# Kernel optimization log

Hardware: AMD Instinct MI355X
Metric: run time of the kernel (lower is better)

The kernel has to match this reference:

```python
import jax, jax.numpy as jnp
import numpy as np

N = 8192
D_IN = 128
D_HID = 256  # hard-coded nn.Linear(input_dim, 256) in the module
D_OUT = 64
BN_EPS = 1e-5
LEAKY_SLOPE = 0.01


def setup_inputs() -> dict:
    key = jax.random.key(0)
    k_h, k_a, k_wt, k_wo = jax.random.split(key, 4)
    H = jax.random.normal(k_h, (N, D_IN), dtype=jnp.float32)
    # Fixed adjacency passed to __init__; values in [0,1) so mask=ceil(A*1e-5) is {0,1}
    A = jax.random.uniform(k_a, (N, N), dtype=jnp.float32)
    bn_weight = jnp.ones((D_IN,), jnp.float32)
    bn_bias = jnp.zeros((D_IN,), jnp.float32)
    W_theta = jax.random.normal(k_wt, (D_IN, D_HID), jnp.float32) * np.float32(1.0 / np.sqrt(D_IN))
    b_theta = jnp.zeros((D_HID,), jnp.float32)
    W_out = jax.random.normal(k_wo, (D_IN, D_OUT), jnp.float32) * np.float32(1.0 / np.sqrt(D_IN))
    b_out = jnp.zeros((D_OUT,), jnp.float32)
    return {"H": H, "A": A, "bn_weight": bn_weight, "bn_bias": bn_bias,
            "W_theta": W_theta, "b_theta": b_theta, "W_out": W_out, "b_out": b_out}


def reference(H, A, bn_weight, bn_bias, W_theta, b_theta, W_out, b_out):
    # BatchNorm1d in training mode: biased batch statistics over the node dim
    mean = jnp.mean(H, axis=0)
    var = jnp.mean(jnp.square(H - mean), axis=0)
    Hn = (H - mean) * jax.lax.rsqrt(var + BN_EPS) * bn_weight + bn_bias  # [N, D_IN]

    Hx = Hn @ W_theta + b_theta  # [N, 256]
    mask = jnp.ceil(A * 1e-5)    # constant {0,1} mask from fixed adjacency

    # Dynamic adjacency: clamp(sigmoid(Hx Hx^T), min=0.1) * mask + I
    S = jnp.clip(jax.nn.sigmoid(Hx @ Hx.T), 0.1, None)  # [N, N]
    Ad = S * mask + jnp.eye(N, dtype=H.dtype)

    # D^{-1/2} A D^{-1/2} via broadcast scaling (same math as diag matmuls)
    d = jax.lax.rsqrt(jnp.sum(Ad, axis=1))  # D^{-0.5}, [N]
    A_hat = Ad * d[:, None] * d[None, :]

    out = A_hat @ (Hn @ W_out + b_out)       # [N, D_OUT]
    out = jnp.where(out >= 0, out, LEAKY_SLOPE * out)  # LeakyReLU(0.01)
    return out, A_hat
```

## Files before the change

### kernel.cpp

```cpp
#include <hip/hip_runtime.h>
#include <hip/hip_bf16.h>

#define N 8192
#define DIN 128
#define DHID 256
#define DOUT 64
#define LDP 72
#define VP 136

typedef __attribute__((ext_vector_type(8))) short short8;
typedef __attribute__((ext_vector_type(8))) unsigned short u16x8;
typedef __attribute__((ext_vector_type(4))) float f32x4;
typedef __attribute__((ext_vector_type(4))) unsigned short u16x4;

typedef __attribute__((address_space(1))) const unsigned int GlbU32;
typedef __attribute__((address_space(3))) unsigned int LdsU32;

__device__ inline void gload16(const void* g, void* l) {
  __builtin_amdgcn_global_load_lds((GlbU32*)g, (LdsU32*)l, 16, 0, 0);
}

#define LGKM_BAR()                                            \
  do {                                                        \
    asm volatile("s_waitcnt lgkmcnt(0)" ::: "memory");        \
    __builtin_amdgcn_sched_barrier(0);                        \
    __builtin_amdgcn_s_barrier();                             \
    __builtin_amdgcn_sched_barrier(0);                        \
  } while (0)

__device__ inline unsigned short f2bf(float x) {
  unsigned u = __float_as_uint(x);
  u += 0x7FFF + ((u >> 16) & 1);
  return (unsigned short)(u >> 16);
}
__device__ inline float bf2f(unsigned short u) {
  return __uint_as_float(((unsigned)u) << 16);
}
__device__ inline float sig_clip(float x) {
  float s = 1.0f / (1.0f + __expf(-x));
  return fmaxf(s, 0.1f);
}

__global__ __launch_bounds__(256) void maskpack(const float* __restrict__ A,
                                                unsigned long long* __restrict__ Mb) {
  size_t i = (size_t)blockIdx.x * 256 + threadIdx.x;
  size_t step = (size_t)gridDim.x * 256;
  int l = threadIdx.x & 63;
  for (; i < (size_t)N * N / 4; i += step) {
    f32x4 a = *(const f32x4*)&A[i * 4];
    unsigned long long b0 = __ballot(a[0] > 0.f);
    unsigned long long b1 = __ballot(a[1] > 0.f);
    unsigned long long b2 = __ballot(a[2] > 0.f);
    unsigned long long b3 = __ballot(a[3] > 0.f);
    size_t g = (i - l) >> 6;
    if (l < 4) {
      unsigned long long bb = (l == 0) ? b0 : (l == 1) ? b1 : (l == 2) ? b2 : b3;
      Mb[g * 4 + l] = bb;
    }
  }
}

__global__ void bn_stats(const float* __restrict__ H, const float* __restrict__ bnw,
                         const float* __restrict__ bnb, float* __restrict__ scale,
                         float* __restrict__ shift) {
  int f = blockIdx.x;
  int t = threadIdx.x;
  float s = 0.f, sq = 0.f;
  for (int r = t; r < N; r += 256) {
    float v = H[(size_t)r * DIN + f];
    s += v; sq += v * v;
  }
  __shared__ float ss[256], s2[256];
  ss[t] = s; s2[t] = sq;
  __syncthreads();
  for (int o = 128; o > 0; o >>= 1) {
    if (t < o) { ss[t] += ss[t + o]; s2[t] += s2[t + o]; }
    __syncthreads();
  }
  if (t == 0) {
    float mean = ss[0] * (1.0f / N);
    float var = s2[0] * (1.0f / N) - mean * mean;
    float sc = rsqrtf(var + 1e-5f) * bnw[f];
    scale[f] = sc;
    shift[f] = bnb[f] - mean * sc;
  }
}

__global__ __launch_bounds__(256) void proj(const float* __restrict__ H,
                     const float* __restrict__ scale, const float* __restrict__ shift,
                     const float* __restrict__ Wt, const float* __restrict__ bt,
                     const float* __restrict__ Wo, const float* __restrict__ bo,
                     unsigned short* __restrict__ Hx, unsigned short* __restrict__ M2T) {
  __shared__ float hn[8][DIN];
  int i0 = blockIdx.x * 8;
  int t = threadIdx.x;
  #pragma unroll
  for (int rep = 0; rep < 4; ++rep) {
    int idx = rep * 256 + t;
    int r = idx >> 7, c = idx & 127;
    float h = H[(size_t)(i0 + r) * DIN + c];
    hn[r][c] = fmaf(h, scale[c], shift[c]);
  }
  __syncthreads();
  {
    int c = t;
    float acc[8];
    float b = bt[c];
    #pragma unroll
    for (int r = 0; r < 8; ++r) acc[r] = b;
    for (int k = 0; k < DIN; ++k) {
      float w = Wt[k * DHID + c];
      #pragma unroll
      for (int r = 0; r < 8; ++r) acc[r] = fmaf(hn[r][k], w, acc[r]);
    }
    #pragma unroll
    for (int r = 0; r < 8; ++r) Hx[(size_t)(i0 + r) * DHID + c] = f2bf(acc[r]);
  }
  if (t < DOUT) {
    int c = t;
    float acc[8];
    float b = bo[c];
    #pragma unroll
    for (int r = 0; r < 8; ++r) acc[r] = b;
    for (int k = 0; k < DIN; ++k) {
      float w = Wo[k * DOUT + c];
      #pragma unroll
      for (int r = 0; r < 8; ++r) acc[r] = fmaf(hn[r][k], w, acc[r]);
    }
    u16x8 v;
    #pragma unroll
    for (int r = 0; r < 8; ++r) v[r] = f2bf(acc[r]);
    *(u16x8*)&M2T[(size_t)c * N + i0] = v;
  }
}

template <int BF16V>
__global__ __launch_bounds__(256) void smat(const unsigned short* __restrict__ Hx,
                     const unsigned long long* __restrict__ Mb,
                     float* __restrict__ rowsum,
                     void* __restrict__ Vout) {
  __shared__ unsigned short lsh[17408];
  __shared__ unsigned mbt32[128][4];
  unsigned short* la = lsh;
  unsigned short* lb = lsh + 8192;
  int jt = blockIdx.x, it = blockIdx.y;
  int i0 = it * 128, j0 = jt * 128;
  int t = threadIdx.x;
  int w = t >> 6, l = t & 63;
  int lr = l & 15, lg = l >> 4;

  if (t < 128) {
    const unsigned long long* src = &Mb[(size_t)(i0 + t) * (N / 64) + (j0 >> 8) * 4];
    int sh = (j0 & 128) ? 32 : 0;
    #pragma unroll
    for (int e = 0; e < 4; ++e)
      mbt32[t][e] = (unsigned)(src[e] >> sh);
  }

  f32x4 acc[2][8];
  f32x4 zero = {0.f, 0.f, 0.f, 0.f};
  #pragma unroll
  for (int m = 0; m < 2; ++m)
    #pragma unroll
    for (int n = 0; n < 8; ++n) acc[m][n] = zero;

  const int srow = l >> 3;
  const int scol = ((l & 7) ^ srow) * 8;
  const int fswz = (lr & 7) * 8;

  for (int c4 = 0; c4 < 4; ++c4) {
    int k0 = c4 * 64;
    __syncthreads();
    #pragma unroll
    for (int rp = 0; rp < 4; ++rp) {
      int chunk = rp * 4 + w;
      int row = chunk * 8 + srow;
      gload16(&Hx[(size_t)(i0 + row) * DHID + k0 + scol], &la[chunk * 512]);
      gload16(&Hx[(size_t)(j0 + row) * DHID + k0 + scol], &lb[chunk * 512]);
    }
    __syncthreads();
    #pragma unroll
    for (int kk = 0; kk < 2; ++kk) {
      int c = (kk * 32 + lg * 8) ^ fswz;
      short8 af[2], bf[8];
      #pragma unroll
      for (int m = 0; m < 2; ++m)
        af[m] = *(const short8*)&la[(w * 32 + m * 16 + lr) * 64 + c];
      #pragma unroll
      for (int n = 0; n < 8; ++n)
        bf[n] = *(const short8*)&lb[(n * 16 + lr) * 64 + c];
      #pragma unroll
      for (int m = 0; m < 2; ++m)
        #pragma unroll
        for (int n = 0; n < 8; ++n)
          acc[m][n] = __builtin_amdgcn_mfma_f32_16x16x32_bf16(af[m], bf[n], acc[m][n], 0, 0, 0);
    }
  }

  if (BF16V) __syncthreads();

  #pragma unroll
  for (int m = 0; m < 2; ++m) {
    #pragma unroll
    for (int r = 0; r < 4; ++r) {
      int rl = w * 32 + m * 16 + lg * 4 + r;
      int gi = i0 + rl;
      unsigned mw = mbt32[rl][lr & 3];
      float part = 0.f;
      #pragma unroll
      for (int n = 0; n < 8; ++n) {
        int gj = j0 + n * 16 + lr;
        float ms = ((mw >> (n * 4 + (lr >> 2))) & 1u) ? 1.f : 0.f;
        float v = sig_clip(acc[m][n][r]) * ms + (gi == gj ? 1.f : 0.f);
        part += v;
        if (BF16V)
          lsh[rl * VP + n * 16 + lr] = f2bf(v);
        else
          ((float*)Vout)[(size_t)gi * N + gj] = v;
      }
      part += __shfl_xor(part, 1);
      part += __shfl_xor(part, 2);
      part += __shfl_xor(part, 4);
      part += __shfl_xor(part, 8);
      if (lr == 0) atomicAdd(&rowsum[gi], part);
    }
  }

  if (BF16V) {
    __syncthreads();
    #pragma unroll
    for (int pass = 0; pass < 8; ++pass) {
      int row = pass * 16 + (t >> 4);
      int cc = (t & 15) * 8;
      u16x8 vv = *(const u16x8*)&lsh[row * VP + cc];
      *(u16x8*)&((unsigned short*)Vout)[(size_t)(i0 + row) * N + j0 + cc] = vv;
    }
  }
}

__global__ void dfin(float* rs) {
  int i = blockIdx.x * 256 + threadIdx.x;
  if (i < N) rs[i] = rsqrtf(rs[i]);
}

template <int BF16V>
__global__ __launch_bounds__(256) void outmm(const void* __restrict__ Vin,
                      const float* __restrict__ dd,
                      const unsigned short* __restrict__ M2T,
                      float* __restrict__ Ahat, float* __restrict__ out) {
  __shared__ unsigned short la[2][128 * LDP];
  int kc = blockIdx.x;
  int it = blockIdx.y;
  int i0 = it * 128;
  int jbase = kc * 512;
  int t = threadIdx.x;
  int w = t >> 6, l = t & 63;
  int lr = l & 15, lg = l >> 4;

  f32x4 acc[2][4];
  f32x4 zero = {0.f, 0.f, 0.f, 0.f};
  #pragma unroll
  for (int m = 0; m < 2; ++m)
    #pragma unroll
    for (int n = 0; n < 4; ++n) acc[m][n] = zero;

  if (BF16V) {
    const unsigned short* V = (const unsigned short*)Vin;
    const int row8 = t >> 3;
    const int cc8 = (t & 7) * 8;

    float di[4];
    #pragma unroll
    for (int rep = 0; rep < 4; ++rep) di[rep] = dd[i0 + rep * 32 + row8];

    u16x8 u[2][4];
    #pragma unroll
    for (int rep = 0; rep < 4; ++rep)
      u[0][rep] = *(const u16x8*)&V[(size_t)(i0 + rep * 32 + row8) * N + jbase + cc8];

    #pragma unroll
    for (int s = 0; s < 8; ++s) {
      const int cur = s & 1;
      const int j0 = jbase + s * 64;
      if (s < 7) {
        #pragma unroll
        for (int rep = 0; rep < 4; ++rep)
          u[cur ^ 1][rep] = *(const u16x8*)&V[(size_t)(i0 + rep * 32 + row8) * N + j0 + 64 + cc8];
      }
      short8 bfr[2][4];
      #pragma unroll
      for (int kk = 0; kk < 2; ++kk)
        #pragma unroll
        for (int n = 0; n < 4; ++n)
          bfr[kk][n] = *(const short8*)&M2T[(size_t)(n * 16 + lr) * N + j0 + kk * 32 + lg * 8];
      f32x4 dj0 = *(const f32x4*)&dd[j0 + cc8];
      f32x4 dj1 = *(const f32x4*)&dd[j0 + cc8 + 4];
      #pragma unroll
      for (int rep = 0; rep < 4; ++rep) {
        int row = rep * 32 + row8;
        size_t idx = (size_t)(i0 + row) * N + j0 + cc8;
        f32x4 s0, s1;
        s0[0] = bf2f(u[cur][rep][0]) * di[rep] * dj0[0];
        s0[1] = bf2f(u[cur][rep][1]) * di[rep] * dj0[1];
        s0[2] = bf2f(u[cur][rep][2]) * di[rep] * dj0[2];
        s0[3] = bf2f(u[cur][rep][3]) * di[rep] * dj0[3];
        s1[0] = bf2f(u[cur][rep][4]) * di[rep] * dj1[0];
        s1[1] = bf2f(u[cur][rep][5]) * di[rep] * dj1[1];
        s1[2] = bf2f(u[cur][rep][6]) * di[rep] * dj1[2];
        s1[3] = bf2f(u[cur][rep][7]) * di[rep] * dj1[3];
        *(f32x4*)&Ahat[idx] = s0;
        *(f32x4*)&Ahat[idx + 4] = s1;
        u16x8 b;
        b[0] = f2bf(s0[0]); b[1] = f2bf(s0[1]); b[2] = f2bf(s0[2]); b[3] = f2bf(s0[3]);
        b[4] = f2bf(s1[0]); b[5] = f2bf(s1[1]); b[6] = f2bf(s1[2]); b[7] = f2bf(s1[3]);
        *(u16x8*)&la[cur][row * LDP + cc8] = b;
      }
      LGKM_BAR();
      #pragma unroll
      for (int kk = 0; kk < 2; ++kk) {
        short8 af[2];
        #pragma unroll
        for (int m = 0; m < 2; ++m)
          af[m] = *(const short8*)&la[cur][(w * 32 + m * 16 + lr) * LDP + kk * 32 + lg * 8];
        #pragma unroll
        for (int m = 0; m < 2; ++m)
          #pragma unroll
          for (int n = 0; n < 4; ++n)
            acc[m][n] = __builtin_amdgcn_mfma_f32_16x16x32_bf16(af[m], bfr[kk][n], acc[m][n], 0, 0, 0);
      }
    }
  } else {
    for (int s = 0; s < 8; ++s) {
      int j0 = jbase + s * 64;
      __syncthreads();
      #pragma unroll
      for (int rep = 0; rep < 8; ++rep) {
        int row = rep * 16 + (t >> 4);
        int cc = (t & 15) * 4;
        size_t idx = (size_t)(i0 + row) * N + j0 + cc;
        f32x4 v = *(const f32x4*)&((const float*)Vin)[idx];
        float dii = dd[i0 + row];
        f32x4 dj = *(const f32x4*)&dd[j0 + cc];
        f32x4 sv;
        sv[0] = v[0] * dii * dj[0]; sv[1] = v[1] * dii * dj[1];
        sv[2] = v[2] * dii * dj[2]; sv[3] = v[3] * dii * dj[3];
        *(f32x4*)&Ahat[idx] = sv;
        u16x4 b;
        b[0] = f2bf(sv[0]); b[1] = f2bf(sv[1]); b[2] = f2bf(sv[2]); b[3] = f2bf(sv[3]);
        *(u16x4*)&la[0][row * LDP + cc] = b;
      }
      __syncthreads();
      #pragma unroll
      for (int kk = 0; kk < 2; ++kk) {
        short8 af[2], bfr[4];
        #pragma unroll
        for (int m = 0; m < 2; ++m)
          af[m] = *(const short8*)&la[0][(w * 32 + m * 16 + lr) * LDP + kk * 32 + lg * 8];
        #pragma unroll
        for (int n = 0; n < 4; ++n)
          bfr[n] = *(const short8*)&M2T[(size_t)(n * 16 + lr) * N + j0 + kk * 32 + lg * 8];
        #pragma unroll
        for (int m = 0; m < 2; ++m)
          #pragma unroll
          for (int n = 0; n < 4; ++n)
            acc[m][n] = __builtin_amdgcn_mfma_f32_16x16x32_bf16(af[m], bfr[n], acc[m][n], 0, 0, 0);
      }
    }
  }

  #pragma unroll
  for (int m = 0; m < 2; ++m)
    #pragma unroll
    for (int n = 0; n < 4; ++n)
      #pragma unroll
      for (int r = 0; r < 4; ++r) {
        int gi = i0 + w * 32 + m * 16 + lg * 4 + r;
        int gc = n * 16 + lr;
        atomicAdd(&out[(size_t)gi * DOUT + gc], acc[m][n][r]);
      }
}

__global__ void leaky(float* out) {
  int i = blockIdx.x * 256 + threadIdx.x;
  if (i < N * DOUT) {
    float x = out[i];
    out[i] = x >= 0.f ? x : 0.01f * x;
  }
}

extern "C" void kernel_launch(void* const* d_in, const int* in_sizes, int n_in,
                              void* d_out, int out_size, void* d_ws, size_t ws_size,
                              hipStream_t stream) {
  const float* H   = (const float*)d_in[0];
  const float* A   = (const float*)d_in[1];
  const float* bnw = (const float*)d_in[2];
  const float* bnb = (const float*)d_in[3];
  const float* Wt  = (const float*)d_in[4];
  const float* bt  = (const float*)d_in[5];
  const float* Wo  = (const float*)d_in[6];
  const float* bo  = (const float*)d_in[7];
  float* out = (float*)d_out;
  float* Ahat = out + (size_t)N * DOUT;

  char* ws = (char*)d_ws;
  float* scale  = (float*)(ws + 0);
  float* shift  = (float*)(ws + 512);
  float* rowsum = (float*)(ws + 4096);
  unsigned short* M2T = (unsigned short*)(ws + 65536);
  unsigned short* Hx  = (unsigned short*)(ws + 2097152);
  unsigned long long* Mb = (unsigned long long*)(ws + (size_t)(6u << 20));
  unsigned short* Vbf = (unsigned short*)(ws + (size_t)(14u << 20));

  const size_t need_bf16 = ((size_t)14 << 20) + (size_t)N * N * 2;
  const bool big = ws_size >= need_bf16;

  hipMemsetAsync(rowsum, 0, N * sizeof(float), stream);
  hipMemsetAsync(out, 0, (size_t)N * DOUT * sizeof(float), stream);

  maskpack<<<4096, 256, 0, stream>>>(A, Mb);
  bn_stats<<<DIN, 256, 0, stream>>>(H, bnw, bnb, scale, shift);
  proj<<<N / 8, 256, 0, stream>>>(H, scale, shift, Wt, bt, Wo, bo, Hx, M2T);
  if (big) {
    smat<1><<<dim3(64, 64), 256, 0, stream>>>(Hx, Mb, rowsum, (void*)Vbf);
    dfin<<<N / 256, 256, 0, stream>>>(rowsum);
    outmm<1><<<dim3(16, 64), 256, 0, stream>>>((const void*)Vbf, rowsum, M2T, Ahat, out);
  } else {
    smat<0><<<dim3(64, 64), 256, 0, stream>>>(Hx, Mb, rowsum, (void*)Ahat);
    dfin<<<N / 256, 256, 0, stream>>>(rowsum);
    outmm<0><<<dim3(16, 64), 256, 0, stream>>>((const void*)Ahat, rowsum, M2T, Ahat, out);
  }
  leaky<<<(N * DOUT + 255) / 256, 256, 0, stream>>>(out);
}
```

Measured before the change: 333.0 us.

## Exploit symmetry of Hx·Hxᵀ to compute only upper-triangle tiles in smat

```diff
diff --git a/kernel.cpp b/kernel.cpp
--- a/kernel.cpp
+++ b/kernel.cpp
@@ -139,15 +139,19 @@
                      const unsigned long long* __restrict__ Mb,
                      float* __restrict__ rowsum,
                      void* __restrict__ Vout) {
+  int jt = blockIdx.x, it = blockIdx.y;
+  if (BF16V && jt < it) return;
   __shared__ unsigned short lsh[17408];
   __shared__ unsigned mbt32[128][4];
+  __shared__ unsigned mbtT[128][4];
+  __shared__ float scs[4][128];
   unsigned short* la = lsh;
   unsigned short* lb = lsh + 8192;
-  int jt = blockIdx.x, it = blockIdx.y;
   int i0 = it * 128, j0 = jt * 128;
   int t = threadIdx.x;
   int w = t >> 6, l = t & 63;
   int lr = l & 15, lg = l >> 4;
+  const bool offdiag = BF16V && (it != jt);
 
   if (t < 128) {
     const unsigned long long* src = &Mb[(size_t)(i0 + t) * (N / 64) + (j0 >> 8) * 4];
@@ -155,6 +159,13 @@
     #pragma unroll
     for (int e = 0; e < 4; ++e)
       mbt32[t][e] = (unsigned)(src[e] >> sh);
+  }
+  if (offdiag && t < 128) {
+    const unsigned long long* srcT = &Mb[(size_t)(j0 + t) * (N / 64) + (i0 >> 8) * 4];
+    int shT = (i0 & 128) ? 32 : 0;
+    #pragma unroll
+    for (int e = 0; e < 4; ++e)
+      mbtT[t][e] = (unsigned)(srcT[e] >> shT);
   }
 
   f32x4 acc[2][8];
@@ -234,6 +245,50 @@
       int cc = (t & 15) * 8;
       u16x8 vv = *(const u16x8*)&lsh[row * VP + cc];
       *(u16x8*)&((unsigned short*)Vout)[(size_t)(i0 + row) * N + j0 + cc] = vv;
+    }
+  }
+
+  if (offdiag) {
+    __syncthreads();
+    float p[8];
+    #pragma unroll
+    for (int n = 0; n < 8; ++n) p[n] = 0.f;
+    #pragma unroll
+    for (int m = 0; m < 2; ++m) {
+      #pragma unroll
+      for (int r = 0; r < 4; ++r) {
+        int rl = w * 32 + m * 16 + lg * 4 + r;
+        int bitp = w * 8 + m * 4 + lg;
+        #pragma unroll
+        for (int n = 0; n < 8; ++n) {
+          int c = n * 16 + lr;
+          float ms = ((mbtT[c][r] >> bitp) & 1u) ? 1.f : 0.f;
+          float v = sig_clip(acc[m][n][r]) * ms;
+          p[n] += v;
+          lsh[c * VP + rl] = f2bf(v);
+        }
+      }
+    }
+    #pragma unroll
+    for (int n = 0; n < 8; ++n) {
+      p[n] += __shfl_xor(p[n], 16);
+      p[n] += __shfl_xor(p[n], 32);
+    }
+    if (lg == 0) {
+      #pragma unroll
+      for (int n = 0; n < 8; ++n) scs[w][n * 16 + lr] = p[n];
+    }
+    __syncthreads();
+    if (t < 128) {
+      float cs = scs[0][t] + scs[1][t] + scs[2][t] + scs[3][t];
+      atomicAdd(&rowsum[j0 + t], cs);
+    }
+    #pragma unroll
+    for (int pass = 0; pass < 8; ++pass) {
+      int row = pass * 16 + (t >> 4);
+      int cc = (t & 15) * 8;
+      u16x8 vv = *(const u16x8*)&lsh[row * VP + cc];
+      *(u16x8*)&((unsigned short*)Vout)[(size_t)(j0 + row) * N + i0 + cc] = vv;
     }
   }
 }
```

Measured after the change: 318.8 us. -4.3%, faster.

## Make smat persistent over eight column tiles with register-resident A fragments and double-buffered B

Applied to the files above, without the earlier changes.

```diff
diff --git a/kernel.cpp b/kernel.cpp
--- a/kernel.cpp
+++ b/kernel.cpp
@@ -12,6 +12,7 @@
 typedef __attribute__((ext_vector_type(8))) unsigned short u16x8;
 typedef __attribute__((ext_vector_type(4))) float f32x4;
 typedef __attribute__((ext_vector_type(4))) unsigned short u16x4;
+typedef __attribute__((ext_vector_type(2))) unsigned long long u64x2;
 
 typedef __attribute__((address_space(1))) const unsigned int GlbU32;
 typedef __attribute__((address_space(3))) unsigned int LdsU32;
@@ -23,6 +24,14 @@
 #define LGKM_BAR()                                            \
   do {                                                        \
     asm volatile("s_waitcnt lgkmcnt(0)" ::: "memory");        \
+    __builtin_amdgcn_sched_barrier(0);                        \
+    __builtin_amdgcn_s_barrier();                             \
+    __builtin_amdgcn_sched_barrier(0);                        \
+  } while (0)
+
+#define VM_BAR(nstr)                                          \
+  do {                                                        \
+    asm volatile("s_waitcnt vmcnt(" nstr ")" ::: "memory");   \
     __builtin_amdgcn_sched_barrier(0);                        \
     __builtin_amdgcn_s_barrier();                             \
     __builtin_amdgcn_sched_barrier(0);                        \
@@ -135,107 +144,171 @@
 }
 
 template <int BF16V>
-__global__ __launch_bounds__(256) void smat(const unsigned short* __restrict__ Hx,
+__global__ __launch_bounds__(256, 2) void smat(const unsigned short* __restrict__ Hx,
                      const unsigned long long* __restrict__ Mb,
                      float* __restrict__ rowsum,
                      void* __restrict__ Vout) {
-  __shared__ unsigned short lsh[17408];
+  __shared__ unsigned short lsh[33792];
   __shared__ unsigned mbt32[128][4];
-  unsigned short* la = lsh;
-  unsigned short* lb = lsh + 8192;
-  int jt = blockIdx.x, it = blockIdx.y;
-  int i0 = it * 128, j0 = jt * 128;
-  int t = threadIdx.x;
-  int w = t >> 6, l = t & 63;
-  int lr = l & 15, lg = l >> 4;
-
-  if (t < 128) {
-    const unsigned long long* src = &Mb[(size_t)(i0 + t) * (N / 64) + (j0 >> 8) * 4];
-    int sh = (j0 & 128) ? 32 : 0;
-    #pragma unroll
-    for (int e = 0; e < 4; ++e)
-      mbt32[t][e] = (unsigned)(src[e] >> sh);
-  }
-
-  f32x4 acc[2][8];
-  f32x4 zero = {0.f, 0.f, 0.f, 0.f};
-  #pragma unroll
-  for (int m = 0; m < 2; ++m)
-    #pragma unroll
-    for (int n = 0; n < 8; ++n) acc[m][n] = zero;
-
+  unsigned short* lb = lsh;
+  unsigned short* lV = lsh + 16384;
+  const int blk = blockIdx.x;
+  const int jb = blk & 7;
+  const int it = blk >> 3;
+  const int i0 = it * 128;
+  const int t = threadIdx.x;
+  const int w = t >> 6, l = t & 63;
+  const int lr = l & 15, lg = l >> 4;
   const int srow = l >> 3;
   const int scol = ((l & 7) ^ srow) * 8;
   const int fswz = (lr & 7) * 8;
 
-  for (int c4 = 0; c4 < 4; ++c4) {
-    int k0 = c4 * 64;
+  short8 af[2][8];
+  #pragma unroll
+  for (int h = 0; h < 2; ++h) {
     __syncthreads();
     #pragma unroll
-    for (int rp = 0; rp < 4; ++rp) {
-      int chunk = rp * 4 + w;
-      int row = chunk * 8 + srow;
-      gload16(&Hx[(size_t)(i0 + row) * DHID + k0 + scol], &la[chunk * 512]);
-      gload16(&Hx[(size_t)(j0 + row) * DHID + k0 + scol], &lb[chunk * 512]);
+    for (int itr = 0; itr < 8; ++itr) {
+      int idx = itr * 4 + w;
+      int c4 = idx >> 3, rg = idx & 7;
+      int row = h * 64 + rg * 8 + srow;
+      gload16(&Hx[(size_t)(i0 + row) * DHID + c4 * 64 + scol], &lsh[idx * 512]);
     }
     __syncthreads();
-    #pragma unroll
-    for (int kk = 0; kk < 2; ++kk) {
-      int c = (kk * 32 + lg * 8) ^ fswz;
-      short8 af[2], bf[8];
-      #pragma unroll
-      for (int m = 0; m < 2; ++m)
-        af[m] = *(const short8*)&la[(w * 32 + m * 16 + lr) * 64 + c];
-      #pragma unroll
-      for (int n = 0; n < 8; ++n)
-        bf[n] = *(const short8*)&lb[(n * 16 + lr) * 64 + c];
-      #pragma unroll
-      for (int m = 0; m < 2; ++m)
+    if ((w >> 1) == h) {
+      #pragma unroll
+      for (int c4 = 0; c4 < 4; ++c4)
+        #pragma unroll
+        for (int kk = 0; kk < 2; ++kk)
+          #pragma unroll
+          for (int m = 0; m < 2; ++m)
+            af[m][c4 * 2 + kk] = *(const short8*)&lsh[c4 * 4096 +
+                ((w & 1) * 32 + m * 16 + lr) * 64 + ((kk * 32 + lg * 8) ^ fswz)];
+    }
+  }
+  __syncthreads();
+
+  {
+    int j0 = jb * 1024;
+    #pragma unroll
+    for (int itr = 0; itr < 4; ++itr) {
+      int rg = itr * 4 + w;
+      int row = rg * 8 + srow;
+      gload16(&Hx[(size_t)(j0 + row) * DHID + scol], &lb[rg * 512]);
+    }
+    int mrow = t >> 1, ep = (t & 1) * 2;
+    u64x2 mv = *(const u64x2*)&Mb[(size_t)(i0 + mrow) * (N / 64) + (j0 >> 8) * 4 + ep];
+    int sh = (j0 & 128) ? 32 : 0;
+    mbt32[mrow][ep] = (unsigned)(mv[0] >> sh);
+    mbt32[mrow][ep + 1] = (unsigned)(mv[1] >> sh);
+  }
+
+  float rs[2][4] = {{0.f, 0.f, 0.f, 0.f}, {0.f, 0.f, 0.f, 0.f}};
+
+  for (int jt = 0; jt < 8; ++jt) {
+    const int j0 = (jb * 8 + jt) * 128;
+    f32x4 acc[2][8];
+    f32x4 zero = {0.f, 0.f, 0.f, 0.f};
+    #pragma unroll
+    for (int m = 0; m < 2; ++m)
+      #pragma unroll
+      for (int n = 0; n < 8; ++n) acc[m][n] = zero;
+
+    #pragma unroll
+    for (int c4 = 0; c4 < 4; ++c4) {
+      bool last = (jt == 7) && (c4 == 3);
+      if (!last) {
+        int njt = (c4 == 3) ? jt + 1 : jt;
+        int nc4 = (c4 == 3) ? 0 : c4 + 1;
+        int nj0 = (jb * 8 + njt) * 128;
+        unsigned short* dst = lb + (((c4 + 1) & 1) * 8192);
+        #pragma unroll
+        for (int itr = 0; itr < 4; ++itr) {
+          int rg = itr * 4 + w;
+          int row = rg * 8 + srow;
+          gload16(&Hx[(size_t)(nj0 + row) * DHID + nc4 * 64 + scol], &dst[rg * 512]);
+        }
+      }
+      if (BF16V) {
+        if (last)            VM_BAR("0");
+        else if (c4 == 0) {
+          if (jt == 0)       VM_BAR("5");
+          else               VM_BAR("13");
+        } else               VM_BAR("4");
+      } else {
+        VM_BAR("0");
+      }
+      const unsigned short* cb = lb + ((c4 & 1) * 8192);
+      #pragma unroll
+      for (int kk = 0; kk < 2; ++kk) {
+        short8 bf[8];
         #pragma unroll
         for (int n = 0; n < 8; ++n)
-          acc[m][n] = __builtin_amdgcn_mfma_f32_16x16x32_bf16(af[m], bf[n], acc[m][n], 0, 0, 0);
-    }
-  }
-
-  if (BF16V) __syncthreads();
+          bf[n] = *(const short8*)&cb[(n * 16 + lr) * 64 + ((kk * 32 + lg * 8) ^ fswz)];
+        #pragma unroll
+        for (int m = 0; m < 2; ++m)
+          #pragma unroll
+          for (int n = 0; n < 8; ++n)
+            acc[m][n] = __builtin_amdgcn_mfma_f32_16x16x32_bf16(af[m][c4 * 2 + kk], bf[n], acc[m][n], 0, 0, 0);
+      }
+      LGKM_BAR();
+    }
+
+    #pragma unroll
+    for (int m = 0; m < 2; ++m) {
+      #pragma unroll
+      for (int r = 0; r < 4; ++r) {
+        int rl = w * 32 + m * 16 + lg * 4 + r;
+        int gi = i0 + rl;
+        unsigned mw = mbt32[rl][lr & 3];
+        float part = 0.f;
+        #pragma unroll
+        for (int n = 0; n < 8; ++n) {
+          int gj = j0 + n * 16 + lr;
+          float ms = ((mw >> (n * 4 + (lr >> 2))) & 1u) ? 1.f : 0.f;
+          float v = sig_clip(acc[m][n][r]) * ms + (gi == gj ? 1.f : 0.f);
+          part += v;
+          if (BF16V)
+            lV[rl * VP + n * 16 + lr] = f2bf(v);
+          else
+            ((float*)Vout)[(size_t)gi * N + gj] = v;
+        }
+        rs[m][r] += part;
+      }
+    }
+    if (BF16V) {
+      LGKM_BAR();
+      #pragma unroll
+      for (int pass = 0; pass < 8; ++pass) {
+        int row = pass * 16 + (t >> 4);
+        int cc2 = (t & 15) * 8;
+        u16x8 vv = *(const u16x8*)&lV[row * VP + cc2];
+        *(u16x8*)&((unsigned short*)Vout)[(size_t)(i0 + row) * N + j0 + cc2] = vv;
+      }
+    } else {
+      __syncthreads();
+    }
+    if (jt < 7) {
+      int nj0 = (jb * 8 + jt + 1) * 128;
+      int mrow = t >> 1, ep = (t & 1) * 2;
+      u64x2 mv = *(const u64x2*)&Mb[(size_t)(i0 + mrow) * (N / 64) + (nj0 >> 8) * 4 + ep];
+      int sh = (nj0 & 128) ? 32 : 0;
+      mbt32[mrow][ep] = (unsigned)(mv[0] >> sh);
+      mbt32[mrow][ep + 1] = (unsigned)(mv[1] >> sh);
+    }
+  }
 
   #pragma unroll
-  for (int m = 0; m < 2; ++m) {
+  for (int m = 0; m < 2; ++m)
     #pragma unroll
     for (int r = 0; r < 4; ++r) {
-      int rl = w * 32 + m * 16 + lg * 4 + r;
-      int gi = i0 + rl;
-      unsigned mw = mbt32[rl][lr & 3];
-      float part = 0.f;
-      #pragma unroll
-      for (int n = 0; n < 8; ++n) {
-        int gj = j0 + n * 16 + lr;
-        float ms = ((mw >> (n * 4 + (lr >> 2))) & 1u) ? 1.f : 0.f;
-        float v = sig_clip(acc[m][n][r]) * ms + (gi == gj ? 1.f : 0.f);
-        part += v;
-        if (BF16V)
-          lsh[rl * VP + n * 16 + lr] = f2bf(v);
-        else
-          ((float*)Vout)[(size_t)gi * N + gj] = v;
-      }
-      part += __shfl_xor(part, 1);
-      part += __shfl_xor(part, 2);
-      part += __shfl_xor(part, 4);
-      part += __shfl_xor(part, 8);
-      if (lr == 0) atomicAdd(&rowsum[gi], part);
-    }
-  }
-
-  if (BF16V) {
-    __syncthreads();
-    #pragma unroll
-    for (int pass = 0; pass < 8; ++pass) {
-      int row = pass * 16 + (t >> 4);
-      int cc = (t & 15) * 8;
-      u16x8 vv = *(const u16x8*)&lsh[row * VP + cc];
-      *(u16x8*)&((unsigned short*)Vout)[(size_t)(i0 + row) * N + j0 + cc] = vv;
-    }
-  }
+      float p = rs[m][r];
+      p += __shfl_xor(p, 1);
+      p += __shfl_xor(p, 2);
+      p += __shfl_xor(p, 4);
+      p += __shfl_xor(p, 8);
+      if (lr == 0) atomicAdd(&rowsum[i0 + w * 32 + m * 16 + lg * 4 + r], p);
+    }
 }
 
 __global__ void dfin(float* rs) {
@@ -421,11 +494,11 @@
   bn_stats<<<DIN, 256, 0, stream>>>(H, bnw, bnb, scale, shift);
   proj<<<N / 8, 256, 0, stream>>>(H, scale, shift, Wt, bt, Wo, bo, Hx, M2T);
   if (big) {
-    smat<1><<<dim3(64, 64), 256, 0, stream>>>(Hx, Mb, rowsum, (void*)Vbf);
+    smat<1><<<512, 256, 0, stream>>>(Hx, Mb, rowsum, (void*)Vbf);
     dfin<<<N / 256, 256, 0, stream>>>(rowsum);
     outmm<1><<<dim3(16, 64), 256, 0, stream>>>((const void*)Vbf, rowsum, M2T, Ahat, out);
   } else {
-    smat<0><<<dim3(64, 64), 256, 0, stream>>>(Hx, Mb, rowsum, (void*)Ahat);
+    smat<0><<<512, 256, 0, stream>>>(Hx, Mb, rowsum, (void*)Ahat);
     dfin<<<N / 256, 256, 0, stream>>>(rowsum);
     outmm<0><<<dim3(16, 64), 256, 0, stream>>>((const void*)Ahat, rowsum, M2T, Ahat, out);
   }
```

New measurement: 323.9 us. 1.03x faster.
